# Performance work log

Measured on AMD Instinct MI355X. Metric: run time of the kernel, lower is better.

## Reference

```python
import jax, jax.numpy as jnp
import numpy as np

EPS = 1e-06
TEMPERATURE = 1.0
RATIO_WEIGHT = 1.0
ENTROPY_WEIGHT = 0.01


def setup_inputs() -> dict:
    key = jax.random.key(0)
    k1, k2, k3 = jax.random.split(key, 3)
    B, N, C, H = 32, 4096, 256, 256
    x = jax.random.normal(k1, (B, N, C), dtype=jnp.float32)
    W1 = jax.random.normal(k2, (C, H), dtype=jnp.float32) * (1.0 / np.sqrt(C))
    b1 = jnp.zeros((H,), dtype=jnp.float32)
    w2 = jax.random.normal(k3, (H,), dtype=jnp.float32) * (1.0 / np.sqrt(H))
    b2 = jnp.zeros((1,), dtype=jnp.float32)
    return {"x": x, "W1": W1, "b1": b1, "w2": w2, "b2": b2, "k": 16}


def reference(x, W1, b1, w2, b2, k):
    # x: [B, N, C] -> soft-mode TokenGater forward
    N = x.shape[-2]
    # MLP scorer: Linear -> GELU(exact) -> Linear -> squeeze(-1)
    h = jax.nn.gelu(jnp.einsum('bnc,ch->bnh', x, W1) + b1, approximate=False)
    scores = jnp.einsum('bnh,h->bn', h, w2) + b2[0]              # [B, N]
    probs = jax.nn.sigmoid(scores / max(TEMPERATURE, EPS))       # [B, N]

    target_ratio = float(k) / float(max(N, 1))
    ratio = probs.mean(axis=-1)                                  # [B]
    loss_ratio = jnp.mean((ratio - target_ratio) ** 2)
    loss_entropy = jnp.mean(-(probs * jnp.log(probs + EPS)
                              + (1.0 - probs) * jnp.log(1.0 - probs + EPS)))
    aux_loss = RATIO_WEIGHT * loss_ratio + ENTROPY_WEIGHT * loss_entropy

    x_keep = x * probs[..., None]                                # [B, N, C]
    bg_w = 1.0 - probs                                           # [B, N]
    denom = jnp.clip(bg_w.sum(axis=-1, keepdims=True), EPS)      # [B, 1]
    bg = jnp.einsum('bnc,bn->bc', x, bg_w) / denom               # [B, C]
    y = jnp.concatenate([x_keep, bg[..., None, :]], axis=-2)     # [B, N+1, C]
    return (y, aux_loss, scores, probs)
```

## Files before the change

### kernel.cpp

```cpp
#include <hip/hip_runtime.h>
#include <cstdint>

#define GEPS 1e-6f

typedef __attribute__((ext_vector_type(8))) short bf16x8;
typedef __attribute__((ext_vector_type(4))) float f32x4;

__device__ __forceinline__ unsigned short f2bf(float f) {
  unsigned int u = __float_as_uint(f);
  u += 0x7fffu + ((u >> 16) & 1u);
  return (unsigned short)(u >> 16);
}

__global__ void pack_w1(const float* __restrict__ W1, unsigned short* __restrict__ wt) {
  int k = blockIdx.x;
  int h = threadIdx.x;
  float v = W1[k * 256 + h];
  int h_tile = h >> 4, tl = h & 15, kk = k >> 5, q = (k >> 3) & 3, j = k & 7;
  wt[(((h_tile << 3) + kk) << 9) + (q << 7) + (tl << 3) + j] = f2bf(v);
}

__global__ __launch_bounds__(256) void gater_main(
    const float* __restrict__ x, const unsigned short* __restrict__ wt,
    const float* __restrict__ b1, const float* __restrict__ w2,
    const float* __restrict__ b2,
    float* __restrict__ y, float* __restrict__ scores, float* __restrict__ probs,
    float* __restrict__ bg_ws, float* __restrict__ sums)
{
  __shared__ short A_lds[64 * 264];
  __shared__ float sc_lds[4][64];
  __shared__ float p_lds[64];
  __shared__ float bg_lds[4][256];

  const int tid = threadIdx.x;
  const int tok0 = blockIdx.x * 64;
  const int b = tok0 >> 12;
  const int n0 = tok0 & 4095;
  const float* xblk = x + (size_t)tok0 * 256;

  #pragma unroll
  for (int i = 0; i < 16; ++i) {
    int f = i * 256 + tid;
    int token = f >> 6;
    int k4 = (f & 63) << 2;
    const float4 v = *(const float4*)(xblk + (size_t)f * 4);
    unsigned int lo = (unsigned int)f2bf(v.x) | ((unsigned int)f2bf(v.y) << 16);
    unsigned int hi = (unsigned int)f2bf(v.z) | ((unsigned int)f2bf(v.w) << 16);
    *(uint2*)&A_lds[token * 264 + k4] = make_uint2(lo, hi);
  }
  __syncthreads();

  const int wave = tid >> 6, lane = tid & 63, tl = lane & 15, q = lane >> 4;

  f32x4 acc[4][4];
  #pragma unroll
  for (int mi = 0; mi < 4; ++mi)
    #pragma unroll
    for (int ni = 0; ni < 4; ++ni)
      acc[mi][ni] = (f32x4){0.f, 0.f, 0.f, 0.f};

  const bf16x8* wtv = (const bf16x8*)wt;
  #pragma unroll
  for (int kk = 0; kk < 8; ++kk) {
    bf16x8 a[4], bb[4];
    #pragma unroll
    for (int mi = 0; mi < 4; ++mi)
      a[mi] = *(const bf16x8*)&A_lds[(mi * 16 + tl) * 264 + kk * 32 + q * 8];
    #pragma unroll
    for (int ni = 0; ni < 4; ++ni)
      bb[ni] = wtv[((((wave << 2) + ni) << 3) + kk) * 64 + lane];
    #pragma unroll
    for (int mi = 0; mi < 4; ++mi)
      #pragma unroll
      for (int ni = 0; ni < 4; ++ni)
        acc[mi][ni] = __builtin_amdgcn_mfma_f32_16x16x32_bf16(a[mi], bb[ni], acc[mi][ni], 0, 0, 0);
  }

  float w2v[4], b1v[4];
  #pragma unroll
  for (int ni = 0; ni < 4; ++ni) {
    int h = wave * 64 + ni * 16 + tl;
    w2v[ni] = w2[h];
    b1v[ni] = b1[h];
  }
  #pragma unroll
  for (int mi = 0; mi < 4; ++mi) {
    #pragma unroll
    for (int r = 0; r < 4; ++r) {
      float s = 0.f;
      #pragma unroll
      for (int ni = 0; ni < 4; ++ni) {
        float hv = acc[mi][ni][r] + b1v[ni];
        float g = 0.5f * hv * (1.0f + erff(hv * 0.70710678118654752f));
        s += g * w2v[ni];
      }
      #pragma unroll
      for (int m = 1; m < 16; m <<= 1) s += __shfl_xor(s, m, 64);
      if (tl == 0) sc_lds[wave][mi * 16 + q * 4 + r] = s;
    }
  }
  __syncthreads();

  if (tid < 64) {
    float s = sc_lds[0][tid] + sc_lds[1][tid] + sc_lds[2][tid] + sc_lds[3][tid] + b2[0];
    float p = 1.0f / (1.0f + expf(-s));
    size_t g = (size_t)tok0 + tid;
    scores[g] = s;
    probs[g] = p;
    p_lds[tid] = p;
    float ent = -(p * logf(p + GEPS) + (1.0f - p) * logf(1.0f - p + GEPS));
    float sp = p, se = ent;
    #pragma unroll
    for (int m = 1; m < 64; m <<= 1) {
      sp += __shfl_xor(sp, m, 64);
      se += __shfl_xor(se, m, 64);
    }
    if (tid == 0) {
      atomicAdd(&sums[b * 2 + 0], sp);
      atomicAdd(&sums[b * 2 + 1], se);
    }
  }
  __syncthreads();

  float4 bg = make_float4(0.f, 0.f, 0.f, 0.f);
  #pragma unroll
  for (int i = 0; i < 16; ++i) {
    int f = i * 256 + tid;
    int token = f >> 6;
    float4 xv = *(const float4*)(xblk + (size_t)f * 4);
    float p = p_lds[token];
    float4 yv = make_float4(xv.x * p, xv.y * p, xv.z * p, xv.w * p);
    size_t row = (size_t)b * 4097 + (size_t)(n0 + token);
    *(float4*)(y + row * 256 + ((f & 63) << 2)) = yv;
    float bw = 1.0f - p;
    bg.x += xv.x * bw; bg.y += xv.y * bw; bg.z += xv.z * bw; bg.w += xv.w * bw;
  }
  *(float4*)&bg_lds[tid >> 6][(tid & 63) << 2] = bg;
  __syncthreads();
  {
    int c = tid;
    float v = bg_lds[0][c] + bg_lds[1][c] + bg_lds[2][c] + bg_lds[3][c];
    atomicAdd(&bg_ws[b * 256 + c], v);
  }
}

__global__ void finalize(const float* __restrict__ bg_ws, const float* __restrict__ sums,
                         const int* __restrict__ kp, float* __restrict__ y,
                         float* __restrict__ aux)
{
  int b = blockIdx.x, c = threadIdx.x;
  float sp = sums[b * 2 + 0];
  float denom = fmaxf(4096.0f - sp, GEPS);
  y[((size_t)b * 4097 + 4096) * 256 + c] = bg_ws[b * 256 + c] / denom;
  if (b == 0 && c == 0) {
    float t = (float)kp[0] / 4096.0f;
    float lr = 0.f, le = 0.f;
    for (int i = 0; i < 32; ++i) {
      float r = sums[i * 2 + 0] / 4096.0f;
      lr += (r - t) * (r - t);
      le += sums[i * 2 + 1];
    }
    aux[0] = lr / 32.0f + 0.01f * (le / (32.0f * 4096.0f));
  }
}

extern "C" void kernel_launch(void* const* d_in, const int* in_sizes, int n_in,
                              void* d_out, int out_size, void* d_ws, size_t ws_size,
                              hipStream_t stream) {
  const float* x  = (const float*)d_in[0];
  const float* W1 = (const float*)d_in[1];
  const float* b1 = (const float*)d_in[2];
  const float* w2 = (const float*)d_in[3];
  const float* b2 = (const float*)d_in[4];
  const int*   kp = (const int*)d_in[5];

  float* y = (float*)d_out;
  const size_t Y_ELEMS = (size_t)32 * 4097 * 256;
  float* aux    = y + Y_ELEMS;
  float* scores = aux + 1;
  float* probs  = scores + (size_t)32 * 4096;

  unsigned short* wt = (unsigned short*)d_ws;
  float* bg_ws = (float*)((char*)d_ws + 131072);
  float* sums  = bg_ws + 32 * 256;

  hipMemsetAsync(bg_ws, 0, (32 * 256 + 64) * sizeof(float), stream);
  pack_w1<<<256, 256, 0, stream>>>(W1, wt);
  gater_main<<<2048, 256, 0, stream>>>(x, wt, b1, w2, b2, y, scores, probs, bg_ws, sums);
  finalize<<<32, 256, 0, stream>>>(bg_ws, sums, kp, y, aux);
}
```

Measured before the change: 316.2 us.

## Swizzle LDS, reuse shared buffer, fast GELU/sigmoid, nontemporal y stores

Replaces the padded A tile with an XOR-swizzled unpadded layout and aliases the score, prob and background scratch onto the same LDS buffer. This cuts shared memory so more blocks fit per CU, and launch bounds now request 5. Exact erff GELU and the expf sigmoid are swapped for an Abramowitz-Stegun polynomial and hardware exp2/rcp approximations, which loosens accuracy. Stores to y become nontemporal and addressing is simplified. An extra barrier is added so the aliased buffer is not overwritten while MFMA reads are still pending.

```diff
diff --git a/kernel.cpp b/kernel.cpp
--- a/kernel.cpp
+++ b/kernel.cpp
@@ -10,6 +10,20 @@
   unsigned int u = __float_as_uint(f);
   u += 0x7fffu + ((u >> 16) & 1u);
   return (unsigned short)(u >> 16);
+}
+
+__device__ __forceinline__ float fast_gelu(float h) {
+  float z  = h * 0.70710678118654752f;
+  float az = __builtin_fabsf(z);
+  float t  = __builtin_amdgcn_rcpf(__builtin_fmaf(0.3275911f, az, 1.0f));
+  float poly = t * __builtin_fmaf(t, __builtin_fmaf(t, __builtin_fmaf(t,
+               __builtin_fmaf(t, 1.061405429f, -1.453152027f),
+               1.421413741f), -0.284496736f), 0.254829592f);
+  float e  = __builtin_amdgcn_exp2f(z * z * -1.44269504088896341f);
+  float er = __builtin_fmaf(-poly, e, 1.0f);
+  er = __builtin_copysignf(er, z);
+  float h5 = 0.5f * h;
+  return __builtin_fmaf(h5, er, h5);
 }
 
 __global__ void pack_w1(const float* __restrict__ W1, unsigned short* __restrict__ wt) {
@@ -20,37 +34,38 @@
   wt[(((h_tile << 3) + kk) << 9) + (q << 7) + (tl << 3) + j] = f2bf(v);
 }
 
-__global__ __launch_bounds__(256) void gater_main(
+__global__ __launch_bounds__(256, 5) void gater_main(
     const float* __restrict__ x, const unsigned short* __restrict__ wt,
     const float* __restrict__ b1, const float* __restrict__ w2,
     const float* __restrict__ b2,
     float* __restrict__ y, float* __restrict__ scores, float* __restrict__ probs,
     float* __restrict__ bg_ws, float* __restrict__ sums)
 {
-  __shared__ short A_lds[64 * 264];
-  __shared__ float sc_lds[4][64];
-  __shared__ float p_lds[64];
-  __shared__ float bg_lds[4][256];
+  __shared__ short A_lds[64 * 256];
+  float* const sc_lds = (float*)A_lds;
+  float* const p_lds  = (float*)A_lds + 256;
+  float* const bg_lds = (float*)A_lds + 320;
 
   const int tid = threadIdx.x;
+  const int wave = tid >> 6;
   const int tok0 = blockIdx.x * 64;
   const int b = tok0 >> 12;
   const int n0 = tok0 & 4095;
   const float* xblk = x + (size_t)tok0 * 256;
+  const float* xt = xblk + tid * 4;
 
   #pragma unroll
   for (int i = 0; i < 16; ++i) {
-    int f = i * 256 + tid;
-    int token = f >> 6;
-    int k4 = (f & 63) << 2;
-    const float4 v = *(const float4*)(xblk + (size_t)f * 4);
+    int token = i * 4 + wave;
+    const float4 v = *(const float4*)(xt + i * 1024);
     unsigned int lo = (unsigned int)f2bf(v.x) | ((unsigned int)f2bf(v.y) << 16);
     unsigned int hi = (unsigned int)f2bf(v.z) | ((unsigned int)f2bf(v.w) << 16);
-    *(uint2*)&A_lds[token * 264 + k4] = make_uint2(lo, hi);
-  }
-  __syncthreads();
-
-  const int wave = tid >> 6, lane = tid & 63, tl = lane & 15, q = lane >> 4;
+    int idx = token * 256 + (((tid & 63) << 2) ^ ((token & 7) << 3));
+    *(uint2*)&A_lds[idx] = make_uint2(lo, hi);
+  }
+  __syncthreads();
+
+  const int lane = tid & 63, tl = lane & 15, q = lane >> 4;
 
   f32x4 acc[4][4];
   #pragma unroll
@@ -60,12 +75,13 @@
       acc[mi][ni] = (f32x4){0.f, 0.f, 0.f, 0.f};
 
   const bf16x8* wtv = (const bf16x8*)wt;
+  const int aswz = (tl & 7) << 3;
   #pragma unroll
   for (int kk = 0; kk < 8; ++kk) {
     bf16x8 a[4], bb[4];
     #pragma unroll
     for (int mi = 0; mi < 4; ++mi)
-      a[mi] = *(const bf16x8*)&A_lds[(mi * 16 + tl) * 264 + kk * 32 + q * 8];
+      a[mi] = *(const bf16x8*)&A_lds[(mi * 16 + tl) * 256 + ((kk * 32 + q * 8) ^ aswz)];
     #pragma unroll
     for (int ni = 0; ni < 4; ++ni)
       bb[ni] = wtv[((((wave << 2) + ni) << 3) + kk) * 64 + lane];
@@ -75,6 +91,7 @@
       for (int ni = 0; ni < 4; ++ni)
         acc[mi][ni] = __builtin_amdgcn_mfma_f32_16x16x32_bf16(a[mi], bb[ni], acc[mi][ni], 0, 0, 0);
   }
+  __syncthreads();
 
   float w2v[4], b1v[4];
   #pragma unroll
@@ -91,19 +108,19 @@
       #pragma unroll
       for (int ni = 0; ni < 4; ++ni) {
         float hv = acc[mi][ni][r] + b1v[ni];
-        float g = 0.5f * hv * (1.0f + erff(hv * 0.70710678118654752f));
-        s += g * w2v[ni];
+        s += fast_gelu(hv) * w2v[ni];
       }
       #pragma unroll
       for (int m = 1; m < 16; m <<= 1) s += __shfl_xor(s, m, 64);
-      if (tl == 0) sc_lds[wave][mi * 16 + q * 4 + r] = s;
+      if (tl == 0) sc_lds[wave * 64 + mi * 16 + q * 4 + r] = s;
     }
   }
   __syncthreads();
 
   if (tid < 64) {
-    float s = sc_lds[0][tid] + sc_lds[1][tid] + sc_lds[2][tid] + sc_lds[3][tid] + b2[0];
-    float p = 1.0f / (1.0f + expf(-s));
+    float s = sc_lds[tid] + sc_lds[64 + tid] + sc_lds[128 + tid] + sc_lds[192 + tid] + b2[0];
+    float e = __builtin_amdgcn_exp2f(s * -1.44269504088896341f);
+    float p = __builtin_amdgcn_rcpf(1.0f + e);
     size_t g = (size_t)tok0 + tid;
     scores[g] = s;
     probs[g] = p;
@@ -122,24 +139,22 @@
   }
   __syncthreads();
 
+  float* const yt = y + ((size_t)b * 4097 + n0) * 256 + tid * 4;
   float4 bg = make_float4(0.f, 0.f, 0.f, 0.f);
   #pragma unroll
   for (int i = 0; i < 16; ++i) {
-    int f = i * 256 + tid;
-    int token = f >> 6;
-    float4 xv = *(const float4*)(xblk + (size_t)f * 4);
-    float p = p_lds[token];
-    float4 yv = make_float4(xv.x * p, xv.y * p, xv.z * p, xv.w * p);
-    size_t row = (size_t)b * 4097 + (size_t)(n0 + token);
-    *(float4*)(y + row * 256 + ((f & 63) << 2)) = yv;
+    float4 xv = *(const float4*)(xt + i * 1024);
+    float p = p_lds[i * 4 + wave];
+    f32x4 yv = {xv.x * p, xv.y * p, xv.z * p, xv.w * p};
+    __builtin_nontemporal_store(yv, (f32x4*)(yt + i * 1024));
     float bw = 1.0f - p;
     bg.x += xv.x * bw; bg.y += xv.y * bw; bg.z += xv.z * bw; bg.w += xv.w * bw;
   }
-  *(float4*)&bg_lds[tid >> 6][(tid & 63) << 2] = bg;
+  *(float4*)&bg_lds[tid * 4] = bg;
   __syncthreads();
   {
     int c = tid;
-    float v = bg_lds[0][c] + bg_lds[1][c] + bg_lds[2][c] + bg_lds[3][c];
+    float v = bg_lds[c] + bg_lds[256 + c] + bg_lds[512 + c] + bg_lds[768 + c];
     atomicAdd(&bg_ws[b * 256 + c], v);
   }
 }
```

New measurement: 339.2 us. 1.07x slower.
